# Kernel tuning notes

Hardware: AMD Instinct MI355X
Metric: run time of the kernel (lower is better)

Reference implementation:

```python
import jax, jax.numpy as jnp
import numpy as np

N = 100000   # nodes
D = 128      # embedding_dim
E = 1600000  # edges (avg in-degree 16)
L = 2        # num_layers
CURV = 1.0   # positive curvature (repo default -1.0 is NaN under sqrt)


def mobius_addition(x, y, c):
    xy = jnp.sum(x * y, axis=-1, keepdims=True)
    xn = jnp.sum(x * x, axis=-1, keepdims=True)
    yn = jnp.sum(y * y, axis=-1, keepdims=True)
    num = (1 + 2 * c * xy + c * yn) * x + (1 - c * xn) * y
    den = 1 + 2 * c * xy + c * c * xn * yn
    return num / den


def exp_map(x, v, c):
    vn = jnp.linalg.norm(v, axis=-1, keepdims=True)
    sc = jnp.sqrt(c)
    second = jnp.tanh(sc * vn / 2) * v / (sc * vn)
    return mobius_addition(x, second, c)


def log_map(x, y, c):
    add = mobius_addition(-x, y, c)
    an = jnp.linalg.norm(add, axis=-1, keepdims=True)
    sc = jnp.sqrt(c)
    return (2 / sc) * jnp.arctanh(sc * an) * add / an


def setup_inputs() -> dict:
    key = jax.random.key(0)
    ks = jax.random.split(key, 10)
    s = 1.0 / np.sqrt(D)  # torch Linear init scale
    embeddings = 0.01 * jax.random.normal(ks[0], (N, D), dtype=jnp.float32)  # ||x||<1 keeps atanh finite
    Wq = jax.random.uniform(ks[1], (L, D, D), jnp.float32, -s, s)
    bq = jax.random.uniform(ks[2], (L, D), jnp.float32, -s, s)
    Wk = jax.random.uniform(ks[3], (L, D, D), jnp.float32, -s, s)
    bk = jax.random.uniform(ks[4], (L, D), jnp.float32, -s, s)
    Wv = jax.random.uniform(ks[5], (L, D, D), jnp.float32, -s, s)
    bv = jax.random.uniform(ks[6], (L, D), jnp.float32, -s, s)
    src = jax.random.randint(ks[7], (E,), 0, N, dtype=jnp.int32)
    # guarantee every node has >=1 in-edge (DGL would leave isolated nodes at h=0 -> exp_map NaN)
    dst = jnp.concatenate([jnp.arange(N, dtype=jnp.int32),
                           jax.random.randint(ks[8], (E - N,), 0, N, dtype=jnp.int32)])
    curvature = jnp.array([CURV], dtype=jnp.float32)
    return {"embeddings": embeddings, "Wq": Wq, "bq": bq, "Wk": Wk, "bk": bk,
            "Wv": Wv, "bv": bv, "curvature": curvature, "src": src, "dst": dst}


def reference(embeddings, Wq, bq, Wk, bk, Wv, bv, curvature, src, dst):
    c = curvature  # shape [1], broadcasts against [..., 1]
    scale = float(D) ** 0.5
    x = embeddings
    origin = jnp.zeros((1, D), dtype=x.dtype)
    for l in range(Wq.shape[0]):
        t = log_map(origin, x, c)                      # [N, D] tangent at origin
        q = t @ Wq[l].T + bq[l]
        k = t @ Wk[l].T + bk[l]
        v = t @ Wv[l].T + bv[l]
        e = jnp.sum(k[src] * q[dst], axis=-1) / scale  # [E] edge scores
        m = jax.ops.segment_max(e, dst, num_segments=N)
        p = jnp.exp(e - m[dst])
        z = jax.ops.segment_sum(p, dst, num_segments=N)
        alpha = p / z[dst]                             # segment softmax over in-edges
        h = jax.ops.segment_sum(alpha[:, None] * v[src], dst, num_segments=N)
        x = exp_map(origin, h, c)
    return x
```

## Files before the change

### kernel.cpp

```cpp
#include <hip/hip_runtime.h>
#include <hip/hip_bf16.h>
#include <stdint.h>

typedef __attribute__((ext_vector_type(8))) short short8;
typedef __attribute__((ext_vector_type(4))) float f32x4;
typedef __attribute__((ext_vector_type(2))) float f32x2;
typedef __attribute__((ext_vector_type(4))) unsigned int u32x4;
typedef __attribute__((ext_vector_type(2))) _Float16 half2_t;

__device__ __forceinline__ uint32_t pack2(float a, float b) {
    auto r = __builtin_amdgcn_cvt_pkrtz(a, b);
    return __builtin_bit_cast(uint32_t, r);
}
__device__ __forceinline__ uint16_t f2h(float x) {
    auto r = __builtin_amdgcn_cvt_pkrtz(x, 0.0f);
    return (uint16_t)(__builtin_bit_cast(uint32_t, r) & 0xffffu);
}

__device__ __forceinline__ void agg_hist_add(int b, int lane, int* lcnt) {
    int prev = __shfl_up(b, 1);
    bool head = (lane == 0) || (b != prev);
    unsigned long long heads = __ballot(head);
    unsigned long long mask_le = ((1ull << lane) << 1) - 1ull;
    unsigned long long g = heads & ~mask_le;
    int nexthead = g ? (int)__builtin_ctzll(g) : 64;
    if (head && b >= 0) atomicAdd(&lcnt[b], nexthead - lane);
}
__device__ __forceinline__ int agg_slot(int b, int lane, int* cnt) {
    int prev = __shfl_up(b, 1);
    bool head = (lane == 0) || (b != prev);
    unsigned long long heads = __ballot(head);
    unsigned long long mask_le = ((1ull << lane) << 1) - 1ull;
    unsigned long long m = heads & mask_le;
    int myhead = 63 - (int)__builtin_clzll(m);
    unsigned long long g = heads & ~mask_le;
    int nexthead = g ? (int)__builtin_ctzll(g) : 64;
    int base = 0;
    if (lane == myhead && b >= 0) base = atomicAdd(&cnt[b], nexthead - lane);
    base = __shfl(base, myhead);
    return base + (lane - myhead);
}

#define DIM 128
#define BKT_SHIFT 7
#define BKT_NODES 128
#define MAX_BKT 1024
#define BIN_TILE 8192
#define CSR_CAP 3072
#define LDS_W_STRIDE 136
#define NW_BLK 16

__global__ __launch_bounds__(256) void prep_kernel(
    const int* __restrict__ dst, int* __restrict__ bucket_cnt, int* __restrict__ done_cnt,
    int* __restrict__ bstart, int* __restrict__ bcursor,
    int E, int nbuckets, int nbin,
    const float* __restrict__ Wq, const float* __restrict__ Wk, const float* __restrict__ Wv,
    uint16_t* __restrict__ w_h, int wtotal,
    const float* __restrict__ x, uint16_t* __restrict__ t, const float* __restrict__ curv,
    int N) {
    __shared__ int lcnt[MAX_BKT];
    __shared__ int is_last;
    int bx = blockIdx.x;
    int tid = threadIdx.x;
    if (bx < nbin) {
        for (int i = tid; i < nbuckets; i += 256) lcnt[i] = 0;
        __syncthreads();
        int base = bx * BIN_TILE;
        int end = min(base + BIN_TILE, E);
        int lane = tid & 63;
        for (int e0 = base; e0 < end; e0 += 256) {
            int e = e0 + tid;
            int b = (e < end) ? (dst[e] >> BKT_SHIFT) : -1;
            agg_hist_add(b, lane, lcnt);
        }
        __syncthreads();
        for (int i = tid; i < nbuckets; i += 256)
            if (lcnt[i]) atomicAdd(&bucket_cnt[i], lcnt[i]);
        if (tid == 0) {
            __threadfence();
            int d = atomicAdd(done_cnt, 1);
            is_last = (d == nbin - 1);
        }
        __syncthreads();
        if (is_last) {
            __threadfence();
            int v4[4];
            #pragma unroll
            for (int c = 0; c < 4; c++) {
                int idx = c * 256 + tid;
                v4[c] = (idx < nbuckets)
                    ? __hip_atomic_load(&bucket_cnt[idx], __ATOMIC_RELAXED, __HIP_MEMORY_SCOPE_AGENT)
                    : 0;
            }
            int run = 0;
            #pragma unroll
            for (int c = 0; c < 4; c++) {
                lcnt[tid] = v4[c]; __syncthreads();
                for (int off = 1; off < 256; off <<= 1) {
                    int tv = (tid >= off) ? lcnt[tid - off] : 0;
                    __syncthreads();
                    lcnt[tid] += tv;
                    __syncthreads();
                }
                int ex = run + lcnt[tid] - v4[c];
                int idx = c * 256 + tid;
                if (idx < nbuckets) { bstart[idx] = ex; bcursor[idx] = ex; }
                run += lcnt[255];
                __syncthreads();
            }
            if (tid == 0) bstart[nbuckets] = E;
        }
    } else if (bx < nbin + NW_BLK) {
        int per_l = 3 * DIM * DIM;
        for (int i = (bx - nbin) * 256 + tid; i < wtotal; i += 256 * NW_BLK) {
            int l = i / per_l;
            int rem = i % per_l;
            int mat = rem / (DIM * DIM);
            int idx = rem % (DIM * DIM);
            const float* s = (mat == 0) ? Wq : (mat == 1) ? Wk : Wv;
            w_h[i] = f2h(s[l * DIM * DIM + idx]);
        }
    } else {
        int n = (bx - nbin - NW_BLK) * 32 + (tid >> 3);
        if (n >= N) return;
        int ln8 = tid & 7;
        const float4* xp = (const float4*)(x + (size_t)n * DIM) + ln8 * 4;
        float4 a0 = xp[0], a1 = xp[1], a2 = xp[2], a3 = xp[3];
        float ss = a0.x * a0.x + a0.y * a0.y + a0.z * a0.z + a0.w * a0.w
                 + a1.x * a1.x + a1.y * a1.y + a1.z * a1.z + a1.w * a1.w
                 + a2.x * a2.x + a2.y * a2.y + a2.z * a2.z + a2.w * a2.w
                 + a3.x * a3.x + a3.y * a3.y + a3.z * a3.z + a3.w * a3.w;
        #pragma unroll
        for (int off = 4; off >= 1; off >>= 1) ss += __shfl_xor(ss, off);
        float c = curv[0];
        float sc = sqrtf(c);
        float r = sqrtf(ss);
        float z = sc * r;
        float f = (r > 1e-30f) ? __logf((1.0f + z) / (1.0f - z)) / (sc * r) : 2.0f;
        uint4 o0, o1;
        o0.x = pack2(f * a0.x, f * a0.y); o0.y = pack2(f * a0.z, f * a0.w);
        o0.z = pack2(f * a1.x, f * a1.y); o0.w = pack2(f * a1.z, f * a1.w);
        o1.x = pack2(f * a2.x, f * a2.y); o1.y = pack2(f * a2.z, f * a2.w);
        o1.z = pack2(f * a3.x, f * a3.y); o1.w = pack2(f * a3.z, f * a3.w);
        uint4* tp = (uint4*)(t + (size_t)n * DIM) + ln8 * 2;
        tp[0] = o0; tp[1] = o1;
    }
}

__global__ __launch_bounds__(256) void bin_kernel(const int* __restrict__ src,
                                                  const int* __restrict__ dst,
                                                  int* __restrict__ bcursor,
                                                  int2* __restrict__ pair_buf,
                                                  int E, int nbuckets) {
    __shared__ int lcnt[MAX_BKT];
    __shared__ int lbase[MAX_BKT];
    int lane = threadIdx.x & 63;
    for (int i = threadIdx.x; i < nbuckets; i += 256) lcnt[i] = 0;
    __syncthreads();
    int base = blockIdx.x * BIN_TILE;
    int end = min(base + BIN_TILE, E);
    for (int e0 = base; e0 < end; e0 += 256) {
        int e = e0 + threadIdx.x;
        int b = (e < end) ? (dst[e] >> BKT_SHIFT) : -1;
        agg_hist_add(b, lane, lcnt);
    }
    __syncthreads();
    for (int i = threadIdx.x; i < nbuckets; i += 256) {
        int c = lcnt[i];
        lbase[i] = c ? atomicAdd(&bcursor[i], c) : 0;
    }
    __syncthreads();
    for (int i = threadIdx.x; i < nbuckets; i += 256) lcnt[i] = 0;
    __syncthreads();
    for (int e0 = base; e0 < end; e0 += 256) {
        int e = e0 + threadIdx.x;
        bool valid = (e < end);
        int d = valid ? dst[e] : 0;
        int b = valid ? (d >> BKT_SHIFT) : -1;
        int slot = agg_slot(b, lane, lcnt);
        if (valid) pair_buf[(size_t)lbase[b] + slot] = make_int2(src[e], d);
    }
}

__global__ __launch_bounds__(256) void csr_kernel(const int2* __restrict__ pair_buf,
                                                  const int* __restrict__ bstart,
                                                  int* __restrict__ row_start,
                                                  int* __restrict__ esrc,
                                                  int N, int E) {
    __shared__ int cnt[BKT_NODES], incl[BKT_NODES], cur[BKT_NODES];
    __shared__ int lsrc[CSR_CAP];
    int b = blockIdx.x;
    int node0 = b << BKT_SHIFT;
    int p0 = bstart[b], p1 = bstart[b + 1];
    int cntb = p1 - p0;
    int tid = threadIdx.x;
    if (tid < BKT_NODES) { cnt[tid] = 0; cur[tid] = 0; }
    __syncthreads();
    for (int i = p0 + tid; i < p1; i += 256)
        atomicAdd(&cnt[pair_buf[i].y & (BKT_NODES - 1)], 1);
    __syncthreads();
    if (tid < BKT_NODES) incl[tid] = cnt[tid];
    __syncthreads();
    for (int off = 1; off < BKT_NODES; off <<= 1) {
        int v = 0;
        if (tid < BKT_NODES && tid >= off) v = incl[tid - off];
        __syncthreads();
        if (tid < BKT_NODES) incl[tid] += v;
        __syncthreads();
    }
    if (tid < BKT_NODES) {
        int n = node0 + tid;
        if (n < N) row_start[n] = p0 + incl[tid] - cnt[tid];
    }
    if (b == 0 && tid == 0) row_start[N] = E;
    bool fit = (cntb <= CSR_CAP);
    __syncthreads();
    for (int i = p0 + tid; i < p1; i += 256) {
        int2 pr = pair_buf[i];
        int ln = pr.y & (BKT_NODES - 1);
        int slot = incl[ln] - cnt[ln] + atomicAdd(&cur[ln], 1);
        if (fit) lsrc[slot] = pr.x;
        else     esrc[p0 + slot] = pr.x;
    }
    __syncthreads();
    if (fit)
        for (int i = tid; i < cntb; i += 256) esrc[p0 + i] = lsrc[i];
}

__global__ __launch_bounds__(256) void qkv_gemm_kernel(
    const uint16_t* __restrict__ t,
    const uint16_t* __restrict__ w,
    const float* __restrict__ bq, const float* __restrict__ bk, const float* __restrict__ bv,
    uint16_t* __restrict__ qout, uint8_t* __restrict__ k8out, uint16_t* __restrict__ vout,
    int N) {
    __shared__ uint16_t lw[DIM * LDS_W_STRIDE];
    int mat = blockIdx.y;
    const uint16_t* wm = w + (size_t)mat * DIM * DIM;
    {
        int r = threadIdx.x >> 1, hf = (threadIdx.x & 1) * 64;
        const uint4* srcp = (const uint4*)(wm + r * DIM + hf);
        uint4* dstp = (uint4*)(lw + r * LDS_W_STRIDE + hf);
        #pragma unroll
        for (int i = 0; i < 8; i++) dstp[i] = srcp[i];
    }
    __syncthreads();
    int wave = threadIdx.x >> 6, lane = threadIdx.x & 63;
    int sub = lane & 15, quad = lane >> 4;
    int node0 = blockIdx.x * 256 + wave * 64;
    const float* bias = (mat == 0) ? bq : (mat == 1) ? bk : bv;
    f32x4 acc[8][4] = {};
    #pragma unroll
    for (int k0 = 0; k0 < DIM; k0 += 32) {
        short8 b[4];
        #pragma unroll
        for (int g = 0; g < 4; g++) {
            int node = node0 + g * 16 + sub;
            int nodec = (node < N) ? node : (N - 1);
            b[g] = *(const short8*)(t + (size_t)nodec * DIM + k0 + quad * 8);
        }
        short8 a[8];
        #pragma unroll
        for (int tile = 0; tile < 8; tile++)
            a[tile] = *(const short8*)(lw + (tile * 16 + sub) * LDS_W_STRIDE + k0 + quad * 8);
        #pragma unroll
        for (int tile = 0; tile < 8; tile++)
            #pragma unroll
            for (int g = 0; g < 4; g++)
                acc[tile][g] = __builtin_amdgcn_mfma_f32_16x16x32_f16(a[tile], b[g], acc[tile][g], 0, 0, 0);
    }
    #pragma unroll
    for (int g = 0; g < 4; g++) {
        int node = node0 + g * 16 + sub;
        if (node >= N) continue;
        if (mat == 1) {
            #pragma unroll
            for (int tile = 0; tile < 8; tile++) {
                float4 bs = *(const float4*)(bias + tile * 16 + quad * 4);
                int pk = 0;
                pk = __builtin_amdgcn_cvt_pk_fp8_f32(acc[tile][g][0] + bs.x, acc[tile][g][1] + bs.y, pk, false);
                pk = __builtin_amdgcn_cvt_pk_fp8_f32(acc[tile][g][2] + bs.z, acc[tile][g][3] + bs.w, pk, true);
                *(uint32_t*)(k8out + (size_t)node * DIM + tile * 16 + quad * 4) = (uint32_t)pk;
            }
        } else {
            uint16_t* outp = (mat == 0) ? qout : vout;
            #pragma unroll
            for (int tile = 0; tile < 8; tile++) {
                float4 bs = *(const float4*)(bias + tile * 16 + quad * 4);
                uint2 pk;
                pk.x = pack2(acc[tile][g][0] + bs.x, acc[tile][g][1] + bs.y);
                pk.y = pack2(acc[tile][g][2] + bs.z, acc[tile][g][3] + bs.w);
                *(uint2*)(outp + (size_t)node * DIM + tile * 16 + quad * 4) = pk;
            }
        }
    }
}

__global__ __launch_bounds__(256) void attn_kernel(
    const uint16_t* __restrict__ q, const uint8_t* __restrict__ k8,
    const uint16_t* __restrict__ v,
    const int* __restrict__ row_start, const int* __restrict__ esrc,
    const float* __restrict__ curv,
    uint16_t* __restrict__ t_out,
    float* __restrict__ x_out,
    int N, int mode) {
    int wave = threadIdx.x >> 6, lane = threadIdx.x & 63;
    int sub = lane & 15, quad = lane >> 4;
    int n = blockIdx.x * 4 + wave;
    if (n >= N) return;
    int s0 = row_start[n], s1 = row_start[n + 1];
    u32x4 qu = __builtin_nontemporal_load((const u32x4*)(q + (size_t)n * DIM + sub * 8));
    f32x2 qf2[4];
    #pragma unroll
    for (int i = 0; i < 4; i++) {
        half2_t qh = __builtin_bit_cast(half2_t, qu[i]);
        qf2[i][0] = (float)qh.x; qf2[i][1] = (float)qh.y;
    }
    const float K2 = 0.12751744154470514f;
    float l = 0.0f;
    half2_t h2[4] = {};
    for (int s = s0; s < s1; s += 64) {
        int idx = s + lane;
        int sidx_all = __builtin_nontemporal_load(esrc + (idx < s1 ? idx : s1 - 1));
        int m = min(16, ((s1 - s) + 3) >> 2);
        for (int it0 = 0; it0 < m; it0 += 4) {
            uint2 ku[4]; uint4 vu[4];
            #pragma unroll
            for (int u = 0; u < 4; u++) {
                int sx = __shfl(sidx_all, (it0 + u) * 4 + quad);
                int ko = sx * DIM + sub * 8;
                ku[u] = *(const uint2*)(k8 + ko);
                vu[u] = *(const uint4*)(v + ko);
            }
            #pragma unroll
            for (int u = 0; u < 4; u++) {
                int e = s + (it0 + u) * 4 + quad;
                bool valid = (e < s1);
                f32x2 d0 = __builtin_amdgcn_cvt_pk_f32_fp8(ku[u].x, false);
                f32x2 d1 = __builtin_amdgcn_cvt_pk_f32_fp8(ku[u].x, true);
                f32x2 d2 = __builtin_amdgcn_cvt_pk_f32_fp8(ku[u].y, false);
                f32x2 d3 = __builtin_amdgcn_cvt_pk_f32_fp8(ku[u].y, true);
                f32x2 acc2 = qf2[0] * d0;
                acc2 += qf2[1] * d1;
                acc2 += qf2[2] * d2;
                acc2 += qf2[3] * d3;
                float dot = acc2[0] + acc2[1];
                #pragma unroll
                for (int off = 8; off >= 1; off >>= 1) dot += __shfl_xor(dot, off);
                float p = valid ? __builtin_amdgcn_exp2f(dot * K2) : 0.0f;
                l += p;
                _Float16 pf = (_Float16)p;
                half2_t ph = {pf, pf};
                #pragma unroll
                for (int i = 0; i < 4; i++) {
                    half2_t vh = __builtin_bit_cast(half2_t, ((const uint32_t*)&vu[u])[i]);
                    h2[i] += ph * vh;
                }
            }
        }
    }
    #pragma unroll
    for (int off = 16; off <= 32; off <<= 1) {
        l += __shfl_xor(l, off);
        #pragma unroll
        for (int i = 0; i < 4; i++) {
            uint32_t hw = __builtin_bit_cast(uint32_t, h2[i]);
            hw = __shfl_xor(hw, off);
            h2[i] += __builtin_bit_cast(half2_t, hw);
        }
    }
    float rl = 1.0f / l;
    if (mode == 0) {
        if (quad == 0) {
            _Float16 rlh = (_Float16)rl;
            half2_t rl2 = {rlh, rlh};
            uint4 pk;
            pk.x = __builtin_bit_cast(uint32_t, h2[0] * rl2);
            pk.y = __builtin_bit_cast(uint32_t, h2[1] * rl2);
            pk.z = __builtin_bit_cast(uint32_t, h2[2] * rl2);
            pk.w = __builtin_bit_cast(uint32_t, h2[3] * rl2);
            *(uint4*)(t_out + (size_t)n * DIM + sub * 8) = pk;
        }
    } else {
        float h[8];
        #pragma unroll
        for (int i = 0; i < 4; i++) {
            h[2 * i]     = (float)h2[i].x * rl;
            h[2 * i + 1] = (float)h2[i].y * rl;
        }
        float ss = 0.0f;
        #pragma unroll
        for (int j = 0; j < 8; j++) ss += h[j] * h[j];
        #pragma unroll
        for (int off = 8; off >= 1; off >>= 1) ss += __shfl_xor(ss, off);
        float c = curv[0];
        float sc = sqrtf(c);
        float nh = sqrtf(ss);
        float f = (nh > 1e-30f) ? tanhf(sc * nh * 0.5f) / (sc * nh) : 0.5f;
        if (quad == 0) {
            f32x4 o0 = {f * h[0], f * h[1], f * h[2], f * h[3]};
            f32x4 o1 = {f * h[4], f * h[5], f * h[6], f * h[7]};
            __builtin_nontemporal_store(o0, (f32x4*)(x_out + (size_t)n * DIM + sub * 8));
            __builtin_nontemporal_store(o1, (f32x4*)(x_out + (size_t)n * DIM + sub * 8 + 4));
        }
    }
}

extern "C" void kernel_launch(void* const* d_in, const int* in_sizes, int n_in,
                              void* d_out, int out_size, void* d_ws, size_t ws_size,
                              hipStream_t stream) {
    const float* emb  = (const float*)d_in[0];
    const float* Wq   = (const float*)d_in[1];
    const float* bq   = (const float*)d_in[2];
    const float* Wk   = (const float*)d_in[3];
    const float* bk   = (const float*)d_in[4];
    const float* Wv   = (const float*)d_in[5];
    const float* bv   = (const float*)d_in[6];
    const float* curv = (const float*)d_in[7];
    const int*   srcp = (const int*)d_in[8];
    const int*   dstp = (const int*)d_in[9];

    const int N = in_sizes[0] / DIM;
    const int L = in_sizes[2] / DIM;
    const int E = in_sizes[8];

    uint8_t* ws = (uint8_t*)d_ws;
    size_t off = 0;
    auto carve = [&](size_t bytes) { size_t o = off; off = (off + bytes + 255) & ~(size_t)255; return o; };
    uint16_t* t_buf   = (uint16_t*)(ws + carve((size_t)N * DIM * 2));
    uint16_t* qb      = (uint16_t*)(ws + carve((size_t)N * DIM * 2));
    uint16_t* vb      = (uint16_t*)(ws + carve((size_t)N * DIM * 2));
    uint8_t*  k8b     = (uint8_t*)(ws + carve((size_t)N * DIM));
    uint16_t* w_h     = (uint16_t*)(ws + carve((size_t)L * 3 * DIM * DIM * 2));
    int* row_start    = (int*)(ws + carve((size_t)(N + 1) * 4));
    int* bucket_cnt   = (int*)(ws + carve((MAX_BKT + 1) * 4));
    int* bstart       = (int*)(ws + carve((MAX_BKT + 1) * 4));
    int* bcursor      = (int*)(ws + carve(MAX_BKT * 4));
    int* esrc         = (int*)(ws + carve((size_t)E * 4));
    (void)ws_size;
    int* done_cnt = bucket_cnt + MAX_BKT;
    int2* pair_buf = (int2*)qb;

    const int nbuckets = (N + BKT_NODES - 1) >> BKT_SHIFT;
    const int nbin = (E + BIN_TILE - 1) / BIN_TILE;
    const int wtotal = L * 3 * DIM * DIM;

    (void)hipMemsetAsync(bucket_cnt, 0, (size_t)(MAX_BKT + 1) * 4, stream);
    int prep_grid = nbin + NW_BLK + (N + 31) / 32;
    prep_kernel<<<prep_grid, 256, 0, stream>>>(dstp, bucket_cnt, done_cnt, bstart, bcursor,
                                               E, nbuckets, nbin,
                                               Wq, Wk, Wv, w_h, wtotal,
                                               emb, t_buf, curv, N);
    bin_kernel<<<nbin, 256, 0, stream>>>(srcp, dstp, bcursor, pair_buf, E, nbuckets);
    csr_kernel<<<nbuckets, 256, 0, stream>>>(pair_buf, bstart, row_start, esrc, N, E);

    dim3 ggrid((N + 255) / 256, 3);
    for (int l = 0; l < L; l++) {
        qkv_gemm_kernel<<<ggrid, 256, 0, stream>>>(
            t_buf, w_h + (size_t)l * 3 * DIM * DIM,
            bq + (size_t)l * DIM, bk + (size_t)l * DIM, bv + (size_t)l * DIM,
            qb, k8b, vb, N);
        int mode = (l == L - 1) ? 1 : 0;
        attn_kernel<<<(N + 3) / 4, 256, 0, stream>>>(
            qb, k8b, vb, row_start, esrc, curv, t_buf, (float*)d_out, N, mode);
    }
}
```

Baseline: 462.0 us.

## Fuse edge binning with first-layer QKV GEMM and deepen attention gather unroll

Merges the edge binning kernel and the layer-0 QKV GEMM into one launch, so binning blocks and GEMM blocks run concurrently and share an LDS buffer. To make this possible, the pair buffer moves from the q buffer into the output buffer, which frees q for the GEMM. The attention gather loop now unrolls by 8 instead of 4 to keep more K/V loads in flight. Risks are higher register pressure in attention and the cost of mixing two different block types within one grid.

```diff
diff --git a/kernel.cpp b/kernel.cpp
--- a/kernel.cpp
+++ b/kernel.cpp
@@ -147,39 +147,123 @@
     }
 }
 
-__global__ __launch_bounds__(256) void bin_kernel(const int* __restrict__ src,
-                                                  const int* __restrict__ dst,
-                                                  int* __restrict__ bcursor,
-                                                  int2* __restrict__ pair_buf,
-                                                  int E, int nbuckets) {
-    __shared__ int lcnt[MAX_BKT];
-    __shared__ int lbase[MAX_BKT];
-    int lane = threadIdx.x & 63;
-    for (int i = threadIdx.x; i < nbuckets; i += 256) lcnt[i] = 0;
-    __syncthreads();
-    int base = blockIdx.x * BIN_TILE;
-    int end = min(base + BIN_TILE, E);
-    for (int e0 = base; e0 < end; e0 += 256) {
-        int e = e0 + threadIdx.x;
-        int b = (e < end) ? (dst[e] >> BKT_SHIFT) : -1;
-        agg_hist_add(b, lane, lcnt);
-    }
-    __syncthreads();
-    for (int i = threadIdx.x; i < nbuckets; i += 256) {
-        int c = lcnt[i];
-        lbase[i] = c ? atomicAdd(&bcursor[i], c) : 0;
-    }
-    __syncthreads();
-    for (int i = threadIdx.x; i < nbuckets; i += 256) lcnt[i] = 0;
-    __syncthreads();
-    for (int e0 = base; e0 < end; e0 += 256) {
-        int e = e0 + threadIdx.x;
-        bool valid = (e < end);
-        int d = valid ? dst[e] : 0;
-        int b = valid ? (d >> BKT_SHIFT) : -1;
-        int slot = agg_slot(b, lane, lcnt);
-        if (valid) pair_buf[(size_t)lbase[b] + slot] = make_int2(src[e], d);
-    }
+__device__ __forceinline__ void qkv_gemm_body(
+    const uint16_t* __restrict__ t, const uint16_t* __restrict__ w,
+    const float* __restrict__ bq, const float* __restrict__ bk, const float* __restrict__ bv,
+    uint16_t* __restrict__ qout, uint8_t* __restrict__ k8out, uint16_t* __restrict__ vout,
+    int N, int mat, int tile, uint16_t* lw) {
+    const uint16_t* wm = w + (size_t)mat * DIM * DIM;
+    {
+        int r = threadIdx.x >> 1, hf = (threadIdx.x & 1) * 64;
+        const uint4* srcp = (const uint4*)(wm + r * DIM + hf);
+        uint4* dstp = (uint4*)(lw + r * LDS_W_STRIDE + hf);
+        #pragma unroll
+        for (int i = 0; i < 8; i++) dstp[i] = srcp[i];
+    }
+    __syncthreads();
+    int wave = threadIdx.x >> 6, lane = threadIdx.x & 63;
+    int sub = lane & 15, quad = lane >> 4;
+    int node0 = tile * 256 + wave * 64;
+    const float* bias = (mat == 0) ? bq : (mat == 1) ? bk : bv;
+    f32x4 acc[8][4] = {};
+    #pragma unroll
+    for (int k0 = 0; k0 < DIM; k0 += 32) {
+        short8 b[4];
+        #pragma unroll
+        for (int g = 0; g < 4; g++) {
+            int node = node0 + g * 16 + sub;
+            int nodec = (node < N) ? node : (N - 1);
+            b[g] = *(const short8*)(t + (size_t)nodec * DIM + k0 + quad * 8);
+        }
+        short8 a[8];
+        #pragma unroll
+        for (int tl = 0; tl < 8; tl++)
+            a[tl] = *(const short8*)(lw + (tl * 16 + sub) * LDS_W_STRIDE + k0 + quad * 8);
+        #pragma unroll
+        for (int tl = 0; tl < 8; tl++)
+            #pragma unroll
+            for (int g = 0; g < 4; g++)
+                acc[tl][g] = __builtin_amdgcn_mfma_f32_16x16x32_f16(a[tl], b[g], acc[tl][g], 0, 0, 0);
+    }
+    #pragma unroll
+    for (int g = 0; g < 4; g++) {
+        int node = node0 + g * 16 + sub;
+        if (node >= N) continue;
+        if (mat == 1) {
+            #pragma unroll
+            for (int tl = 0; tl < 8; tl++) {
+                float4 bs = *(const float4*)(bias + tl * 16 + quad * 4);
+                int pk = 0;
+                pk = __builtin_amdgcn_cvt_pk_fp8_f32(acc[tl][g][0] + bs.x, acc[tl][g][1] + bs.y, pk, false);
+                pk = __builtin_amdgcn_cvt_pk_fp8_f32(acc[tl][g][2] + bs.z, acc[tl][g][3] + bs.w, pk, true);
+                *(uint32_t*)(k8out + (size_t)node * DIM + tl * 16 + quad * 4) = (uint32_t)pk;
+            }
+        } else {
+            uint16_t* outp = (mat == 0) ? qout : vout;
+            #pragma unroll
+            for (int tl = 0; tl < 8; tl++) {
+                float4 bs = *(const float4*)(bias + tl * 16 + quad * 4);
+                uint2 pk;
+                pk.x = pack2(acc[tl][g][0] + bs.x, acc[tl][g][1] + bs.y);
+                pk.y = pack2(acc[tl][g][2] + bs.z, acc[tl][g][3] + bs.w);
+                *(uint2*)(outp + (size_t)node * DIM + tl * 16 + quad * 4) = pk;
+            }
+        }
+    }
+}
+
+__global__ __launch_bounds__(256) void bin_gemm_kernel(
+    const int* __restrict__ src, const int* __restrict__ dst,
+    int* __restrict__ bcursor, int2* __restrict__ pair_buf, int E, int nbuckets, int nbin,
+    const uint16_t* __restrict__ t, const uint16_t* __restrict__ w,
+    const float* __restrict__ bq, const float* __restrict__ bk, const float* __restrict__ bv,
+    uint16_t* __restrict__ qout, uint8_t* __restrict__ k8out, uint16_t* __restrict__ vout,
+    int N, int ntiles) {
+    __shared__ uint16_t lw[DIM * LDS_W_STRIDE];
+    int bx = blockIdx.x;
+    if (bx < nbin) {
+        int* lcnt = (int*)lw;
+        int* lbase = lcnt + MAX_BKT;
+        int lane = threadIdx.x & 63;
+        for (int i = threadIdx.x; i < nbuckets; i += 256) lcnt[i] = 0;
+        __syncthreads();
+        int base = bx * BIN_TILE;
+        int end = min(base + BIN_TILE, E);
+        for (int e0 = base; e0 < end; e0 += 256) {
+            int e = e0 + threadIdx.x;
+            int b = (e < end) ? (dst[e] >> BKT_SHIFT) : -1;
+            agg_hist_add(b, lane, lcnt);
+        }
+        __syncthreads();
+        for (int i = threadIdx.x; i < nbuckets; i += 256) {
+            int c = lcnt[i];
+            lbase[i] = c ? atomicAdd(&bcursor[i], c) : 0;
+        }
+        __syncthreads();
+        for (int i = threadIdx.x; i < nbuckets; i += 256) lcnt[i] = 0;
+        __syncthreads();
+        for (int e0 = base; e0 < end; e0 += 256) {
+            int e = e0 + threadIdx.x;
+            bool valid = (e < end);
+            int d = valid ? dst[e] : 0;
+            int b = valid ? (d >> BKT_SHIFT) : -1;
+            int slot = agg_slot(b, lane, lcnt);
+            if (valid) pair_buf[(size_t)lbase[b] + slot] = make_int2(src[e], d);
+        }
+    } else {
+        int id = bx - nbin;
+        int mat = id / ntiles, tile = id % ntiles;
+        qkv_gemm_body(t, w, bq, bk, bv, qout, k8out, vout, N, mat, tile, lw);
+    }
+}
+
+__global__ __launch_bounds__(256) void qkv_gemm_kernel(
+    const uint16_t* __restrict__ t, const uint16_t* __restrict__ w,
+    const float* __restrict__ bq, const float* __restrict__ bk, const float* __restrict__ bv,
+    uint16_t* __restrict__ qout, uint8_t* __restrict__ k8out, uint16_t* __restrict__ vout,
+    int N) {
+    __shared__ uint16_t lw[DIM * LDS_W_STRIDE];
+    qkv_gemm_body(t, w, bq, bk, bv, qout, k8out, vout, N, blockIdx.y, blockIdx.x, lw);
 }
 
 __global__ __launch_bounds__(256) void csr_kernel(const int2* __restrict__ pair_buf,
@@ -225,74 +309,6 @@
     __syncthreads();
     if (fit)
         for (int i = tid; i < cntb; i += 256) esrc[p0 + i] = lsrc[i];
-}
-
-__global__ __launch_bounds__(256) void qkv_gemm_kernel(
-    const uint16_t* __restrict__ t,
-    const uint16_t* __restrict__ w,
-    const float* __restrict__ bq, const float* __restrict__ bk, const float* __restrict__ bv,
-    uint16_t* __restrict__ qout, uint8_t* __restrict__ k8out, uint16_t* __restrict__ vout,
-    int N) {
-    __shared__ uint16_t lw[DIM * LDS_W_STRIDE];
-    int mat = blockIdx.y;
-    const uint16_t* wm = w + (size_t)mat * DIM * DIM;
-    {
-        int r = threadIdx.x >> 1, hf = (threadIdx.x & 1) * 64;
-        const uint4* srcp = (const uint4*)(wm + r * DIM + hf);
-        uint4* dstp = (uint4*)(lw + r * LDS_W_STRIDE + hf);
-        #pragma unroll
-        for (int i = 0; i < 8; i++) dstp[i] = srcp[i];
-    }
-    __syncthreads();
-    int wave = threadIdx.x >> 6, lane = threadIdx.x & 63;
-    int sub = lane & 15, quad = lane >> 4;
-    int node0 = blockIdx.x * 256 + wave * 64;
-    const float* bias = (mat == 0) ? bq : (mat == 1) ? bk : bv;
-    f32x4 acc[8][4] = {};
-    #pragma unroll
-    for (int k0 = 0; k0 < DIM; k0 += 32) {
-        short8 b[4];
-        #pragma unroll
-        for (int g = 0; g < 4; g++) {
-            int node = node0 + g * 16 + sub;
-            int nodec = (node < N) ? node : (N - 1);
-            b[g] = *(const short8*)(t + (size_t)nodec * DIM + k0 + quad * 8);
-        }
-        short8 a[8];
-        #pragma unroll
-        for (int tile = 0; tile < 8; tile++)
-            a[tile] = *(const short8*)(lw + (tile * 16 + sub) * LDS_W_STRIDE + k0 + quad * 8);
-        #pragma unroll
-        for (int tile = 0; tile < 8; tile++)
-            #pragma unroll
-            for (int g = 0; g < 4; g++)
-                acc[tile][g] = __builtin_amdgcn_mfma_f32_16x16x32_f16(a[tile], b[g], acc[tile][g], 0, 0, 0);
-    }
-    #pragma unroll
-    for (int g = 0; g < 4; g++) {
-        int node = node0 + g * 16 + sub;
-        if (node >= N) continue;
-        if (mat == 1) {
-            #pragma unroll
-            for (int tile = 0; tile < 8; tile++) {
-                float4 bs = *(const float4*)(bias + tile * 16 + quad * 4);
-                int pk = 0;
-                pk = __builtin_amdgcn_cvt_pk_fp8_f32(acc[tile][g][0] + bs.x, acc[tile][g][1] + bs.y, pk, false);
-                pk = __builtin_amdgcn_cvt_pk_fp8_f32(acc[tile][g][2] + bs.z, acc[tile][g][3] + bs.w, pk, true);
-                *(uint32_t*)(k8out + (size_t)node * DIM + tile * 16 + quad * 4) = (uint32_t)pk;
-            }
-        } else {
-            uint16_t* outp = (mat == 0) ? qout : vout;
-            #pragma unroll
-            for (int tile = 0; tile < 8; tile++) {
-                float4 bs = *(const float4*)(bias + tile * 16 + quad * 4);
-                uint2 pk;
-                pk.x = pack2(acc[tile][g][0] + bs.x, acc[tile][g][1] + bs.y);
-                pk.y = pack2(acc[tile][g][2] + bs.z, acc[tile][g][3] + bs.w);
-                *(uint2*)(outp + (size_t)node * DIM + tile * 16 + quad * 4) = pk;
-            }
-        }
-    }
 }
 
 __global__ __launch_bounds__(256) void attn_kernel(
@@ -322,17 +338,17 @@
         int idx = s + lane;
         int sidx_all = __builtin_nontemporal_load(esrc + (idx < s1 ? idx : s1 - 1));
         int m = min(16, ((s1 - s) + 3) >> 2);
-        for (int it0 = 0; it0 < m; it0 += 4) {
-            uint2 ku[4]; uint4 vu[4];
-            #pragma unroll
-            for (int u = 0; u < 4; u++) {
+        for (int it0 = 0; it0 < m; it0 += 8) {
+            uint2 ku[8]; uint4 vu[8];
+            #pragma unroll
+            for (int u = 0; u < 8; u++) {
                 int sx = __shfl(sidx_all, (it0 + u) * 4 + quad);
                 int ko = sx * DIM + sub * 8;
                 ku[u] = *(const uint2*)(k8 + ko);
                 vu[u] = *(const uint4*)(v + ko);
             }
             #pragma unroll
-            for (int u = 0; u < 4; u++) {
+            for (int u = 0; u < 8; u++) {
                 int e = s + (it0 + u) * 4 + quad;
                 bool valid = (e < s1);
                 f32x2 d0 = __builtin_amdgcn_cvt_pk_f32_fp8(ku[u].x, false);
@@ -438,11 +454,12 @@
     int* esrc         = (int*)(ws + carve((size_t)E * 4));
     (void)ws_size;
     int* done_cnt = bucket_cnt + MAX_BKT;
-    int2* pair_buf = (int2*)qb;
+    int2* pair_buf = (int2*)d_out;
 
     const int nbuckets = (N + BKT_NODES - 1) >> BKT_SHIFT;
     const int nbin = (E + BIN_TILE - 1) / BIN_TILE;
     const int wtotal = L * 3 * DIM * DIM;
+    const int ntiles = (N + 255) / 256;
 
     (void)hipMemsetAsync(bucket_cnt, 0, (size_t)(MAX_BKT + 1) * 4, stream);
     int prep_grid = nbin + NW_BLK + (N + 31) / 32;
@@ -450,11 +467,15 @@
                                                E, nbuckets, nbin,
                                                Wq, Wk, Wv, w_h, wtotal,
                                                emb, t_buf, curv, N);
-    bin_kernel<<<nbin, 256, 0, stream>>>(srcp, dstp, bcursor, pair_buf, E, nbuckets);
+    bin_gemm_kernel<<<nbin + 3 * ntiles, 256, 0, stream>>>(
+        srcp, dstp, bcursor, pair_buf, E, nbuckets, nbin,
+        t_buf, w_h, bq, bk, bv, qb, k8b, vb, N, ntiles);
     csr_kernel<<<nbuckets, 256, 0, stream>>>(pair_buf, bstart, row_start, esrc, N, E);
 
-    dim3 ggrid((N + 255) / 256, 3);
-    for (int l = 0; l < L; l++) {
+    attn_kernel<<<(N + 3) / 4, 256, 0, stream>>>(
+        qb, k8b, vb, row_start, esrc, curv, t_buf, (float*)d_out, N, (L == 1) ? 1 : 0);
+    dim3 ggrid(ntiles, 3);
+    for (int l = 1; l < L; l++) {
         qkv_gemm_kernel<<<ggrid, 256, 0, stream>>>(
             t_buf, w_h + (size_t)l * 3 * DIM * DIM,
             bq + (size_t)l * DIM, bk + (size_t)l * DIM, bv + (size_t)l * DIM,
```

After: 476.6 us. +3.2%, slower.
